# Optimization experiments

Hardware: AMD Instinct MI355X
Metric: run time of the kernel (lower is better)

The kernel has to match this reference:

```python
import jax, jax.numpy as jnp
import numpy as np

B, T, E, H, VF, C = 4, 8192, 512, 8, 2, 256
KD = E // H          # key dim per head = 64
HD = E * VF // H     # value head dim = 128


def _rel_pos():
    decay = np.log(1.0 - 2.0 ** (-5.0 - np.arange(H, dtype=np.float64)))  # [H]
    ang = 1.0 / (10000 ** np.linspace(0, 1, KD // 2))
    ang = np.repeat(ang, 2)                                  # [KD]
    idx = np.arange(T)
    sin = np.sin(idx[:, None] * ang[None, :]).astype(np.float32)
    cos = np.cos(idx[:, None] * ang[None, :]).astype(np.float32)
    bi = np.arange(C)
    diff = bi[:, None] - bi[None, :]
    m = np.where(diff >= 0, np.exp(decay[:, None, None] * diff), 0.0)  # [H,C,C]
    last = m[:, -1]                                          # [H,C]
    vid = (last / last.sum(-1, keepdims=True))[:, :, None]   # [H,C,1]
    scale = np.sqrt(m.sum(-1, keepdims=True))                # [H,C,1]
    mask = (m / scale).astype(np.float32)
    cross_decay = np.exp(decay * C)[:, None, None].astype(np.float32)  # [H,1,1]
    qid = np.exp(decay[:, None] * (bi + 1))[:, :, None]      # [H,C,1]
    qid = (qid / (scale / last.sum(-1)[:, None, None])).astype(np.float32)
    return sin, cos, mask, cross_decay, qid, vid.astype(np.float32)


def setup_inputs() -> dict:
    key = jax.random.key(0)
    ks = jax.random.split(key, 6)
    sin, cos, mask, cross_decay, qid, vid = _rel_pos()
    s = 0.02
    return {
        'x': jax.random.normal(ks[0], (B, T, E), jnp.float32),
        'sin': jnp.asarray(sin), 'cos': jnp.asarray(cos),
        'mask': jnp.asarray(mask), 'cross_decay': jnp.asarray(cross_decay),
        'query_inner_decay': jnp.asarray(qid), 'value_inner_decay': jnp.asarray(vid),
        'Wq': jax.random.normal(ks[1], (E, E), jnp.float32) * s,
        'Wk': jax.random.normal(ks[2], (E, E), jnp.float32) * s,
        'Wv': jax.random.normal(ks[3], (E, E * VF), jnp.float32) * s,
        'Wg': jax.random.normal(ks[4], (E, E * VF), jnp.float32) * s,
        'Wo': jax.random.normal(ks[5], (E * VF, E), jnp.float32) * s,
    }


def _rotate_every_two(x):
    x1, x2 = x[..., ::2], x[..., 1::2]
    return jnp.stack((-x2, x1), axis=-1).reshape(x.shape)


def _theta_shift(x, sin, cos):
    return x * cos + _rotate_every_two(x) * sin


def reference(x, sin, cos, mask, cross_decay, query_inner_decay, value_inner_decay, Wq, Wk, Wv, Wg, Wo):
    Bz, Tl, _ = x.shape
    q = (x @ Wq).reshape(Bz, Tl, H, KD).transpose(0, 2, 1, 3)               # [B,H,T,KD]
    k = ((x @ Wk) * (KD ** -0.5)).reshape(Bz, Tl, H, KD).transpose(0, 2, 1, 3)
    v = x @ Wv                                                              # [B,T,E*VF]
    g = x @ Wg
    qr = _theta_shift(q, sin, cos)
    kr = _theta_shift(k, sin, cos)

    NC = Tl // C
    qr = qr.reshape(Bz, H, NC, C, KD).transpose(0, 2, 1, 3, 4)              # [B,NC,H,C,KD]
    kr = kr.reshape(Bz, H, NC, C, KD).transpose(0, 2, 1, 3, 4)
    vc = v.reshape(Bz, NC, C, H, HD).transpose(0, 1, 3, 2, 4)               # [B,NC,H,C,HD]

    qk = jnp.einsum('bnhck,bnhdk->bnhcd', qr, kr) * mask                    # decay-masked intra-chunk
    inner_scale = jnp.clip(jax.lax.stop_gradient(jnp.abs(qk)).sum(-1, keepdims=True), 1.0, None)
    qk = qk / inner_scale
    inner_output = jnp.einsum('bnhcd,bnhde->bnhce', qk, vc)                 # [B,NC,H,C,HD]

    kv = jnp.einsum('bnhck,bnhcd->bnhkd', kr, vc * value_inner_decay)       # [B,NC,H,KD,HD]

    def step(carry, kv_i):
        kv_state, kv_scale = carry
        out = (kv_state / kv_scale, kv_scale)
        kv_state = kv_state * cross_decay + kv_i
        kv_scale = jnp.clip(
            jax.lax.stop_gradient(jnp.abs(kv_state)).sum(-2, keepdims=True).max(-1, keepdims=True),
            1.0, None)
        return (kv_state, kv_scale), out

    kv_state0 = jnp.zeros((Bz, H, KD, HD), x.dtype)
    kv_scale0 = jnp.ones((Bz, H, 1, 1), x.dtype)
    _, (kv_recurrent, cross_scale) = jax.lax.scan(step, (kv_state0, kv_scale0), jnp.swapaxes(kv, 0, 1))
    kv_recurrent = jnp.swapaxes(kv_recurrent, 0, 1)                         # [B,NC,H,KD,HD]
    cross_scale = jnp.swapaxes(cross_scale, 0, 1)                           # [B,NC,H,1,1]

    all_scale = jnp.maximum(inner_scale, cross_scale)
    cross_output = jnp.einsum('bnhck,bnhkd->bnhcd', qr * query_inner_decay, kv_recurrent)
    output = inner_output / (all_scale / inner_scale) + cross_output / (all_scale / cross_scale)
    output = output.transpose(0, 1, 3, 2, 4)                                # [B,NC,C,H,HD]
    # group_norm: RMSNorm over head_dim, no affine
    output = output * jax.lax.rsqrt(jnp.mean(output ** 2, -1, keepdims=True) + 1e-6)
    output = output.reshape(Bz, Tl, H * HD)
    output = jax.nn.silu(g) * output
    return output @ Wo
```

## Files before the change

### kernel.cpp

```cpp
#include <hip/hip_runtime.h>
#include <cmath>

#define Bz 4
#define Tt 8192
#define Ee 512
#define Hh 8
#define Cc 256
#define KD 64
#define HD 128
#define NC 32
#define EV 1024
#define Mrows (Bz*Tt)

typedef unsigned short u16;
typedef __attribute__((ext_vector_type(4))) float f32x4;
typedef __attribute__((ext_vector_type(8))) short s16x8;

__device__ __forceinline__ u16 f2b(float f) {
    union { float f; unsigned u; } v; v.f = f;
    unsigned r = v.u + 0x7FFFu + ((v.u >> 16) & 1u);
    return (u16)(r >> 16);
}
__device__ __forceinline__ float b2f(u16 u) {
    union { unsigned u; float f; } v; v.u = ((unsigned)u) << 16;
    return v.f;
}
#define MFMA16(a, b, c) __builtin_amdgcn_mfma_f32_16x16x32_bf16((a), (b), (c), 0, 0, 0)

__device__ __forceinline__ void glds16(const u16* g, u16* l) {
    __builtin_amdgcn_global_load_lds(
        (const __attribute__((address_space(1))) unsigned int*)g,
        (__attribute__((address_space(3))) unsigned int*)l,
        16, 0, 0);
}

__device__ __forceinline__ size_t fpk(int row, int k, int K) {
    return (size_t)(row >> 4) * (K * 16) + (k >> 5) * 512 + ((k >> 3) & 3) * 128 +
           (row & 15) * 8 + (k & 7);
}

__global__ __launch_bounds__(256) void cast_x_k(const float* __restrict__ x,
                                                u16* __restrict__ xb) {
    size_t i = ((size_t)blockIdx.x * 256 + threadIdx.x) * 4;
    float4 v = *(const float4*)(x + i);
    int m = (int)(i >> 9), e = (int)(i & 511);
    ushort4 o;
    o.x = f2b(v.x); o.y = f2b(v.y); o.z = f2b(v.z); o.w = f2b(v.w);
    *(ushort4*)(xb + fpk(m, e, 512)) = o;
}

__global__ __launch_bounds__(256) void castT_k(const float* __restrict__ W,
                                               u16* __restrict__ Wt,
                                               int K, int N, float scale) {
    __shared__ float tile[32][33];
    int k0 = blockIdx.y * 32, n0 = blockIdx.x * 32;
    int r = threadIdx.x >> 3, c4 = (threadIdx.x & 7) * 4;
    float4 v = *(const float4*)(W + (size_t)(k0 + r) * N + n0 + c4);
    tile[r][c4] = v.x; tile[r][c4 + 1] = v.y; tile[r][c4 + 2] = v.z; tile[r][c4 + 3] = v.w;
    __syncthreads();
    ushort4 o;
    o.x = f2b(tile[c4 + 0][r] * scale);
    o.y = f2b(tile[c4 + 1][r] * scale);
    o.z = f2b(tile[c4 + 2][r] * scale);
    o.w = f2b(tile[c4 + 3][r] * scale);
    *(ushort4*)(Wt + fpk(n0 + r, k0 + c4, K)) = o;
}

template <int EPI>
__global__ __launch_bounds__(256) void gemm_mfma(const u16* __restrict__ A,
                                                 const u16* __restrict__ Bt,
                                                 void* __restrict__ Cout,
                                                 int K, int N,
                                                 const float* __restrict__ sn,
                                                 const float* __restrict__ cs) {
    __shared__ __align__(16) u16 pool[20480];
    u16 (*lds)[8192] = (u16(*)[8192])pool;
    int tid = threadIdx.x;
    int lane = tid & 63, wid = tid >> 6;
    int cL = lane & 15, quad = lane >> 4;
    int M0 = blockIdx.y * 8, N0 = blockIdx.x * 8;
    int m0 = blockIdx.y * 128 + (wid & 1) * 64;
    int n0 = blockIdx.x * 128 + (wid >> 1) * 64;
    const int KT = K * 16;
    const int NK = K >> 5;

#define STAGE(buf, kc) do {                                                        \
        size_t kofs = (size_t)(kc) * 512 + lane * 8;                               \
        glds16(A  + (size_t)(M0 + wid * 2    ) * KT + kofs,                        \
               &lds[buf][(wid * 2    ) * 512]);                                    \
        glds16(A  + (size_t)(M0 + wid * 2 + 1) * KT + kofs,                        \
               &lds[buf][(wid * 2 + 1) * 512]);                                    \
        glds16(Bt + (size_t)(N0 + wid * 2    ) * KT + kofs,                        \
               &lds[buf][4096 + (wid * 2    ) * 512]);                             \
        glds16(Bt + (size_t)(N0 + wid * 2 + 1) * KT + kofs,                        \
               &lds[buf][4096 + (wid * 2 + 1) * 512]);                             \
    } while (0)

    STAGE(0, 0);
    __syncthreads();

    f32x4 acc[4][4] = {};
    int mh = (wid & 1) * 4, nh = (wid >> 1) * 4;
    for (int kc = 0; kc < NK; ++kc) {
        int cur = kc & 1;
        if (kc + 1 < NK) STAGE(cur ^ 1, kc + 1);
        s16x8 af[4], bfr[4];
        int fo = quad * 128 + cL * 8;
        #pragma unroll
        for (int mt = 0; mt < 4; ++mt)
            af[mt] = *(const s16x8*)(&lds[cur][(mh + mt) * 512 + fo]);
        #pragma unroll
        for (int nt = 0; nt < 4; ++nt)
            bfr[nt] = *(const s16x8*)(&lds[cur][4096 + (nh + nt) * 512 + fo]);
        #pragma unroll
        for (int mt = 0; mt < 4; ++mt)
            #pragma unroll
            for (int nt = 0; nt < 4; ++nt)
                acc[mt][nt] = MFMA16(af[mt], bfr[nt], acc[mt][nt]);
        __syncthreads();
    }
#undef STAGE
    u16* ep = pool + wid * 5120;

    if (EPI == 0) {
        u16* dst = (u16*)Cout;
        int b = m0 >> 13, h = n0 >> 6, tb = m0 & 8191;
        #pragma unroll
        for (int mt = 0; mt < 4; ++mt)
            #pragma unroll
            for (int nt = 0; nt < 4; ++nt)
                #pragma unroll
                for (int i = 0; i < 4; ++i) {
                    int mrow = mt * 16 + quad * 4 + i;
                    int n = n0 + nt * 16 + cL;
                    float v = acc[mt][nt][i];
                    float p = __shfl_xor(v, 1, 64);
                    int t = tb + mrow, kd = n & 63;
                    float c1 = cs[t * 64 + kd], s1 = sn[t * 64 + kd];
                    float o = (n & 1) ? (v * c1 + p * s1) : (v * c1 - p * s1);
                    ep[mrow * 80 + nt * 16 + cL] = f2b(o);
                }
        u16* dstbh = dst + (size_t)(b * 8 + h) * 524288;
        #pragma unroll
        for (int g2 = 0; g2 < 4; ++g2)
            #pragma unroll
            for (int pass = 0; pass < 2; ++pass) {
                int kcol = pass * 32 + quad * 8;
                s16x8 vv = *(const s16x8*)(ep + (g2 * 16 + cL) * 80 + kcol);
                *(s16x8*)(dstbh + fpk(tb + g2 * 16 + cL, kcol, 64)) = vv;
            }
    } else if (EPI == 1) {
        u16* vt = (u16*)Cout;
        #pragma unroll
        for (int mt = 0; mt < 4; ++mt)
            #pragma unroll
            for (int nt = 0; nt < 4; ++nt) {
                int m = m0 + mt * 16 + quad * 4;
                int n = n0 + nt * 16 + cL;
                int b = m >> 13, t = m & 8191;
                int nn = t >> 8, ccc = t & 255;
                int h = n >> 7, e = n & 127;
                ushort4 pk;
                pk.x = f2b(acc[mt][nt][0]);
                pk.y = f2b(acc[mt][nt][1]);
                pk.z = f2b(acc[mt][nt][2]);
                pk.w = f2b(acc[mt][nt][3]);
                *(ushort4*)(vt + (((size_t)((b * 8 + h) * 32 + nn)) << 15) +
                            fpk(e, ccc, 256)) = pk;
            }
    } else if (EPI == 2) {
        u16* dst = (u16*)Cout;
        #pragma unroll
        for (int mt = 0; mt < 4; ++mt)
            #pragma unroll
            for (int nt = 0; nt < 4; ++nt)
                #pragma unroll
                for (int i = 0; i < 4; ++i)
                    ep[(mt * 16 + quad * 4 + i) * 80 + nt * 16 + cL] =
                        f2b(acc[mt][nt][i]);
        #pragma unroll
        for (int g2 = 0; g2 < 4; ++g2)
            #pragma unroll
            for (int pass = 0; pass < 2; ++pass) {
                int ncol = pass * 32 + quad * 8;
                s16x8 vv = *(const s16x8*)(ep + (g2 * 16 + cL) * 80 + ncol);
                *(s16x8*)(dst + fpk(m0 + g2 * 16 + cL, n0 + ncol, N)) = vv;
            }
    } else {
        float* dst = (float*)Cout;
        #pragma unroll
        for (int mt = 0; mt < 4; ++mt)
            #pragma unroll
            for (int nt = 0; nt < 4; ++nt)
                #pragma unroll
                for (int i = 0; i < 4; ++i)
                    dst[(size_t)(m0 + mt * 16 + quad * 4 + i) * N + n0 + nt * 16 + cL] =
                        acc[mt][nt][i];
    }
}

__global__ __launch_bounds__(256) void attn_mfma(const u16* __restrict__ qr,
                                                 const u16* __restrict__ kr,
                                                 const u16* __restrict__ vt,
                                                 const float* __restrict__ mask,
                                                 u16* __restrict__ ATT,
                                                 float* __restrict__ iscale_g) {
    __shared__ __align__(16) u16 Ss[64][264];
    __shared__ float partial[4][64];
    __shared__ float sInvL[64];
    int p = blockIdx.x;
    int g = (p & 7) | ((p >> 5) << 3);
    int rtile = (p >> 3) & 3;
    int h = g & 7; int n = (g >> 3) & 31; int b = g >> 8;
    int tid = threadIdx.x, lane = tid & 63, w = tid >> 6;
    int cL = lane & 15, quad = lane >> 4;

    size_t qf_bh = (size_t)(b * 8 + h) * 524288;
    f32x4 acc[4][4] = {};
    if (w <= rtile) {
        const u16* Qb = qr + qf_bh + (size_t)(n * 16 + rtile * 4) * 1024;
        const u16* Kb = kr + qf_bh + (size_t)(n * 16 + w * 4) * 1024;
        #pragma unroll
        for (int kt = 0; kt < 2; ++kt) {
            s16x8 af[4], bfr[4];
            size_t ko = (size_t)kt * 512 + quad * 128 + cL * 8;
            #pragma unroll
            for (int mt = 0; mt < 4; ++mt)
                af[mt] = *(const s16x8*)(Qb + (size_t)mt * 1024 + ko);
            #pragma unroll
            for (int nt = 0; nt < 4; ++nt)
                bfr[nt] = *(const s16x8*)(Kb + (size_t)nt * 1024 + ko);
            #pragma unroll
            for (int mt = 0; mt < 4; ++mt)
                #pragma unroll
                for (int nt = 0; nt < 4; ++nt)
                    acc[mt][nt] = MFMA16(af[mt], bfr[nt], acc[mt][nt]);
        }
    }
    float rs[4][4] = {};
    if (w <= rtile) {
        const float* mb = mask + ((size_t)h << 16);
        #pragma unroll
        for (int mt = 0; mt < 4; ++mt)
            #pragma unroll
            for (int nt = 0; nt < 4; ++nt)
                #pragma unroll
                for (int i = 0; i < 4; ++i) {
                    int r = rtile * 64 + mt * 16 + quad * 4 + i;
                    int d = w * 64 + nt * 16 + cL;
                    float s = acc[mt][nt][i] * mb[r * 256 + d];
                    Ss[mt * 16 + quad * 4 + i][w * 64 + nt * 16 + cL] = f2b(s);
                    rs[mt][i] += fabsf(s);
                }
    }
    #pragma unroll
    for (int mt = 0; mt < 4; ++mt)
        #pragma unroll
        for (int i = 0; i < 4; ++i) {
            float v = rs[mt][i];
            v += __shfl_xor(v, 1, 16);
            v += __shfl_xor(v, 2, 16);
            v += __shfl_xor(v, 4, 16);
            v += __shfl_xor(v, 8, 16);
            if (cL == 0) partial[w][mt * 16 + quad * 4 + i] = v;
        }
    __syncthreads();
    if (tid < 64) {
        float tot = partial[0][tid] + partial[1][tid] + partial[2][tid] + partial[3][tid];
        tot = fmaxf(tot, 1.f);
        iscale_g[((size_t)((b * 32 + n) * 8 + h)) * 256 + rtile * 64 + tid] = tot;
        sInvL[tid] = 1.f / tot;
    }
    __syncthreads();

    f32x4 o[8] = {};
    const u16* Vb = vt + (((size_t)((b * 8 + h) * 32 + n)) << 15);
    int kmax = 2 * (rtile + 1);
    for (int kt = 0; kt < kmax; ++kt) {
        s16x8 a = *(const s16x8*)(&Ss[w * 16 + cL][kt * 32 + quad * 8]);
        #pragma unroll
        for (int nt = 0; nt < 8; ++nt) {
            s16x8 bv = *(const s16x8*)(Vb + (size_t)nt * 4096 + kt * 512 +
                                       quad * 128 + cL * 8);
            o[nt] = MFMA16(a, bv, o[nt]);
        }
    }
    #pragma unroll
    for (int nt = 0; nt < 8; ++nt)
        #pragma unroll
        for (int i = 0; i < 4; ++i) {
            int r = quad * 4 + i;
            Ss[w * 16 + r][nt * 16 + cL] = f2b(o[nt][i] * sInvL[w * 16 + r]);
        }
    size_t obase = ((size_t)b * 8192 + n * 256 + rtile * 64) * 1024 + h * 128;
    #pragma unroll
    for (int pass = 0; pass < 4; ++pass) {
        int e = pass * 32 + quad * 8;
        s16x8 vv = *(const s16x8*)(&Ss[w * 16 + cL][e]);
        *(s16x8*)(ATT + obase + (size_t)(w * 16 + cL) * 1024 + e) = vv;
    }
}

__global__ __launch_bounds__(256) void chunkkv_mfma(const u16* __restrict__ kr,
                                                    const u16* __restrict__ vt,
                                                    const float* __restrict__ vid,
                                                    float* __restrict__ kvT) {
    __shared__ u16 KtL[64][264];
    int bid = blockIdx.x;
    int h = bid & 7; bid >>= 3;
    int n = bid & 31; int b = bid >> 5;
    int tid = threadIdx.x, lane = tid & 63, w = tid >> 6;
    int cL = lane & 15, quad = lane >> 4;
    size_t qf_bh = (size_t)(b * 8 + h) * 524288;
    {
        int c = tid;
        const u16* rp = kr + qf_bh + (size_t)(n * 16 + (c >> 4)) * 1024 + (c & 15) * 8;
        #pragma unroll
        for (int u = 0; u < 8; ++u) {
            s16x8 vv = *(const s16x8*)(rp + (u >> 2) * 512 + (u & 3) * 128);
            #pragma unroll
            for (int j = 0; j < 8; ++j) KtL[u * 8 + j][c] = (u16)vv[j];
        }
    }
    __syncthreads();
    const u16* Vb = vt + (((size_t)((b * 8 + h) * 32 + n)) << 15);
    f32x4 acc[2][4] = {};
    for (int kt = 0; kt < 8; ++kt) {
        float vidv[8];
        #pragma unroll
        for (int j = 0; j < 8; ++j) vidv[j] = vid[h * 256 + kt * 32 + quad * 8 + j];
        s16x8 af[2];
        #pragma unroll
        for (int mt = 0; mt < 2; ++mt) {
            s16x8 raw = *(const s16x8*)(Vb + (size_t)(w * 2 + mt) * 4096 +
                                        kt * 512 + quad * 128 + cL * 8);
            #pragma unroll
            for (int j = 0; j < 8; ++j)
                af[mt][j] = (short)f2b(b2f((u16)raw[j]) * vidv[j]);
        }
        #pragma unroll
        for (int nt = 0; nt < 4; ++nt) {
            s16x8 bv = *(const s16x8*)(&KtL[nt * 16 + cL][kt * 32 + quad * 8]);
            #pragma unroll
            for (int mt = 0; mt < 2; ++mt) acc[mt][nt] = MFMA16(af[mt], bv, acc[mt][nt]);
        }
    }
    float* out = kvT + ((size_t)((b * 32 + n) * 8 + h)) * 8192;
    #pragma unroll
    for (int mt = 0; mt < 2; ++mt)
        #pragma unroll
        for (int nt = 0; nt < 4; ++nt)
            #pragma unroll
            for (int i = 0; i < 4; ++i)
                out[(w * 32 + mt * 16 + quad * 4 + i) * 64 + nt * 16 + cL] = acc[mt][nt][i];
}

__global__ __launch_bounds__(256) void scan_par(const float* __restrict__ kvT,
                                                u16* __restrict__ kvrecb,
                                                const float* __restrict__ cdv,
                                                float* __restrict__ cscale) {
    int bid = blockIdx.x;
    int n = bid & 31; bid >>= 5;
    int h = bid & 7; int b = bid >> 3;
    int tid = threadIdx.x, lane = tid & 63, g = tid >> 6;
    float cd = cdv[h];
    float st[32];
    #pragma unroll
    for (int i = 0; i < 32; ++i) st[i] = 0.f;
    for (int j = 0; j < n; ++j) {
        size_t base = ((size_t)((b * 32 + j) * 8 + h)) * 8192;
        #pragma unroll
        for (int i = 0; i < 32; ++i) {
            int e = g + 4 * i;
            st[i] = st[i] * cd + kvT[base + e * 64 + lane];
        }
    }
    __shared__ float esum[128];
    __shared__ float sSc;
    #pragma unroll
    for (int i = 0; i < 32; ++i) {
        float s = fabsf(st[i]);
        s += __shfl_xor(s, 1, 64);
        s += __shfl_xor(s, 2, 64);
        s += __shfl_xor(s, 4, 64);
        s += __shfl_xor(s, 8, 64);
        s += __shfl_xor(s, 16, 64);
        s += __shfl_xor(s, 32, 64);
        if (lane == 0) esum[g + 4 * i] = s;
    }
    __syncthreads();
    if (tid < 64) {
        float m1 = fmaxf(esum[tid], esum[tid + 64]);
        m1 = fmaxf(m1, __shfl_xor(m1, 1, 64));
        m1 = fmaxf(m1, __shfl_xor(m1, 2, 64));
        m1 = fmaxf(m1, __shfl_xor(m1, 4, 64));
        m1 = fmaxf(m1, __shfl_xor(m1, 8, 64));
        m1 = fmaxf(m1, __shfl_xor(m1, 16, 64));
        m1 = fmaxf(m1, __shfl_xor(m1, 32, 64));
        if (tid == 0) sSc = fmaxf(m1, 1.f);
    }
    __syncthreads();
    float scale = sSc;
    float inv = 1.f / scale;
    size_t baseN = ((size_t)((b * 32 + n) * 8 + h)) * 8192;
    #pragma unroll
    for (int i = 0; i < 32; ++i) {
        int e = g + 4 * i;
        kvrecb[baseN + ((size_t)(lane >> 3) * 128 + e) * 8 + (lane & 7)] = f2b(st[i] * inv);
    }
    if (tid == 0) cscale[(b * 32 + n) * 8 + h] = scale;
}

__global__ __launch_bounds__(256) void cross_mfma(const u16* __restrict__ qr,
                                                  const u16* __restrict__ kvrecb,
                                                  const float* __restrict__ iscale_g,
                                                  const float* __restrict__ cscale_g,
                                                  const float* __restrict__ qid,
                                                  u16* __restrict__ ATT) {
    __shared__ __align__(16) u16 X[4][4608];
    int bid = blockIdx.x;
    int h = bid & 7; bid >>= 3;
    int n = bid & 31; int b = bid >> 5;
    int tid = threadIdx.x, lane = tid & 63, w = tid >> 6;
    int cL = lane & 15, quad = lane >> 4;
    size_t qf_bh = (size_t)(b * 8 + h) * 524288;
    const u16* Qb = qr + qf_bh + (size_t)(n * 16 + w * 4) * 1024;
    const u16* KVb = kvrecb + ((size_t)((b * 32 + n) * 8 + h)) * 8192;
    s16x8 af[4][2];
    #pragma unroll
    for (int mt = 0; mt < 4; ++mt)
        #pragma unroll
        for (int kt = 0; kt < 2; ++kt)
            af[mt][kt] = *(const s16x8*)(Qb + (size_t)mt * 1024 + kt * 512 +
                                         quad * 128 + cL * 8);
    float csc = cscale_g[(b * 32 + n) * 8 + h];
    size_t ibase = ((size_t)((b * 32 + n) * 8 + h)) * 256 + w * 64;
    size_t obase = ((size_t)(b * 8192 + n * 256 + w * 64)) * 1024 + h * 128;
    #pragma unroll
    for (int hn = 0; hn < 2; ++hn) {
        f32x4 acc[4][4] = {};
        #pragma unroll
        for (int kt = 0; kt < 2; ++kt)
            #pragma unroll
            for (int nt = 0; nt < 4; ++nt) {
                int e = (hn * 4 + nt) * 16 + cL;
                s16x8 bv = *(const s16x8*)(KVb + ((size_t)(kt * 4 + quad) * 128 + e) * 8);
                #pragma unroll
                for (int mt = 0; mt < 4; ++mt)
                    acc[mt][nt] = MFMA16(af[mt][kt], bv, acc[mt][nt]);
            }
        #pragma unroll
        for (int mt = 0; mt < 4; ++mt)
            #pragma unroll
            for (int i = 0; i < 4; ++i) {
                int r = mt * 16 + quad * 4 + i;
                float isc = iscale_g[ibase + r];
                float alls = fmaxf(isc, csc);
                float fC = (csc / alls) * qid[h * 256 + w * 64 + r];
                #pragma unroll
                for (int nt = 0; nt < 4; ++nt)
                    X[w][r * 72 + nt * 16 + cL] = f2b(acc[mt][nt][i] * fC);
            }
        #pragma unroll
        for (int g2 = 0; g2 < 4; ++g2)
            #pragma unroll
            for (int pass = 0; pass < 2; ++pass) {
                int r2 = g2 * 16 + cL;
                float isc2 = iscale_g[ibase + r2];
                float fI2 = isc2 / fmaxf(isc2, csc);
                int e = pass * 32 + quad * 8;
                s16x8 sv = *(const s16x8*)(&X[w][r2 * 72 + e]);
                size_t oi = obase + (size_t)r2 * 1024 + hn * 64 + e;
                s16x8 pv = *(const s16x8*)(ATT + oi);
                s16x8 ov;
                #pragma unroll
                for (int j = 0; j < 8; ++j)
                    ov[j] = (short)f2b(b2f((u16)pv[j]) * fI2 + b2f((u16)sv[j]));
                *(s16x8*)(ATT + oi) = ov;
            }
    }
}

__global__ __launch_bounds__(256) void rms_silu(const u16* __restrict__ ATT,
                                                u16* __restrict__ g) {
    __shared__ u16 att_s[16 * 1036];
    __shared__ float rmsv[16][8];
    int tile = blockIdx.x;
    int tid = threadIdx.x;
    size_t abase = (size_t)tile * 16 * 1024;
    int head = tid >> 5;
    #pragma unroll
    for (int jj = 0; jj < 16; ++jj) {
        ushort4 v = *(const ushort4*)(ATT + abase + (size_t)jj * 1024 + tid * 4);
        *(ushort4*)(att_s + jj * 1036 + tid * 4) = v;
        float x0 = b2f(v.x), x1 = b2f(v.y), x2 = b2f(v.z), x3 = b2f(v.w);
        float ss = x0 * x0 + x1 * x1 + x2 * x2 + x3 * x3;
        ss += __shfl_xor(ss, 1, 32);
        ss += __shfl_xor(ss, 2, 32);
        ss += __shfl_xor(ss, 4, 32);
        ss += __shfl_xor(ss, 8, 32);
        ss += __shfl_xor(ss, 16, 32);
        if ((tid & 31) == 0)
            rmsv[jj][head] = rsqrtf(ss * (1.f / 128.f) + 1e-6f);
    }
    __syncthreads();
    size_t gbase = (size_t)tile * 16384;
    #pragma unroll
    for (int it = 0; it < 16; ++it) {
        int p = it * 1024 + tid * 4;
        int e = ((p >> 9) << 5) | (((p >> 7) & 3) << 3) | (p & 7);
        int r = (p >> 3) & 15;
        ushort4 gv = *(const ushort4*)(g + gbase + p);
        ushort4 av = *(const ushort4*)(att_s + r * 1036 + e);
        float rms = rmsv[r][e >> 7];
        float x0 = b2f(av.x), x1 = b2f(av.y), x2 = b2f(av.z), x3 = b2f(av.w);
        float g0 = b2f(gv.x), g1 = b2f(gv.y), g2 = b2f(gv.z), g3 = b2f(gv.w);
        ushort4 ov;
        ov.x = f2b((g0 / (1.f + __expf(-g0))) * x0 * rms);
        ov.y = f2b((g1 / (1.f + __expf(-g1))) * x1 * rms);
        ov.z = f2b((g2 / (1.f + __expf(-g2))) * x2 * rms);
        ov.w = f2b((g3 / (1.f + __expf(-g3))) * x3 * rms);
        *(ushort4*)(g + gbase + p) = ov;
    }
}

extern "C" void kernel_launch(void* const* d_in, const int* in_sizes, int n_in,
                              void* d_out, int out_size, void* d_ws, size_t ws_size,
                              hipStream_t stream) {
    const float* x    = (const float*)d_in[0];
    const float* sn   = (const float*)d_in[1];
    const float* cs   = (const float*)d_in[2];
    const float* mask = (const float*)d_in[3];
    const float* cdv  = (const float*)d_in[4];
    const float* qid  = (const float*)d_in[5];
    const float* vid  = (const float*)d_in[6];
    const float* Wq   = (const float*)d_in[7];
    const float* Wk   = (const float*)d_in[8];
    const float* Wv   = (const float*)d_in[9];
    const float* Wg   = (const float*)d_in[10];
    const float* Wo   = (const float*)d_in[11];
    float* out = (float*)d_out;

    char* w = (char*)d_ws;
    u16* qr     = (u16*)w;   w += (size_t)16777216 * 2;
    u16* kr     = (u16*)w;   w += (size_t)16777216 * 2;
    u16* vt     = (u16*)w;   w += (size_t)33554432 * 2;
    u16* xbf    = (u16*)w;   w += (size_t)16777216 * 2;
    u16* wqT    = (u16*)w;   w += (size_t)262144 * 2;
    u16* wkT    = (u16*)w;   w += (size_t)262144 * 2;
    u16* wvT    = (u16*)w;   w += (size_t)524288 * 2;
    u16* wgT    = (u16*)w;   w += (size_t)524288 * 2;
    u16* woT    = (u16*)w;   w += (size_t)524288 * 2;
    float* kvT  = (float*)w; w += (size_t)8388608 * 4;
    u16* kvrecb = (u16*)w;   w += (size_t)8388608 * 2;
    float* iscale = (float*)w; w += (size_t)262144 * 4;
    float* cscale = (float*)w; w += (size_t)1024 * 4;

    u16* gbuf = qr;
    u16* ATT  = (u16*)d_out;

    dim3 blk(256);
    cast_x_k<<<dim3(16384), blk, 0, stream>>>(x, xbf);
    castT_k<<<dim3(16, 16), blk, 0, stream>>>(Wq, wqT, 512, 512, 1.0f);
    castT_k<<<dim3(16, 16), blk, 0, stream>>>(Wk, wkT, 512, 512, 0.125f);
    castT_k<<<dim3(32, 16), blk, 0, stream>>>(Wv, wvT, 512, 1024, 1.0f);
    castT_k<<<dim3(32, 16), blk, 0, stream>>>(Wg, wgT, 512, 1024, 1.0f);
    castT_k<<<dim3(16, 32), blk, 0, stream>>>(Wo, woT, 1024, 512, 1.0f);
    gemm_mfma<0><<<dim3(4, 256), blk, 0, stream>>>(xbf, wqT, qr, 512, 512, sn, cs);
    gemm_mfma<0><<<dim3(4, 256), blk, 0, stream>>>(xbf, wkT, kr, 512, 512, sn, cs);
    gemm_mfma<1><<<dim3(8, 256), blk, 0, stream>>>(xbf, wvT, vt, 512, 1024, nullptr, nullptr);
    attn_mfma<<<dim3(4096), blk, 0, stream>>>(qr, kr, vt, mask, ATT, iscale);
    chunkkv_mfma<<<dim3(1024), blk, 0, stream>>>(kr, vt, vid, kvT);
    scan_par<<<dim3(1024), blk, 0, stream>>>(kvT, kvrecb, cdv, cscale);
    cross_mfma<<<dim3(1024), blk, 0, stream>>>(qr, kvrecb, iscale, cscale, qid, ATT);
    gemm_mfma<2><<<dim3(8, 256), blk, 0, stream>>>(xbf, wgT, gbuf, 512, 1024, nullptr, nullptr);
    rms_silu<<<dim3(2048), blk, 0, stream>>>(ATT, gbuf);
    gemm_mfma<3><<<dim3(4, 256), blk, 0, stream>>>(gbuf, woT, out, 1024, 512, nullptr, nullptr);
}
```

Measured before the change: 647.3 us.

## Fuse RMSNorm+SiLU gating into gate GEMM epilogue, bf16 mask, prefetch scan loads

Removes the separate rms_silu kernel by computing the per-head RMS normalization and SiLU gating inside the Wg GEMM epilogue, staging the gate tile through LDS. This avoids writing and re-reading the gate buffer. The mask is also pre-cast to bf16 so attention reads half the bytes, and the scan kernel software-prefetches the next chunk's state. These add an extra cast kernel, some mask precision loss, and more registers in the scan kernel.

```diff
diff --git a/kernel.cpp b/kernel.cpp
--- a/kernel.cpp
+++ b/kernel.cpp
@@ -49,6 +49,15 @@
     *(ushort4*)(xb + fpk(m, e, 512)) = o;
 }
 
+__global__ __launch_bounds__(256) void cast_mask_k(const float* __restrict__ m,
+                                                   u16* __restrict__ mb) {
+    size_t i = ((size_t)blockIdx.x * 256 + threadIdx.x) * 4;
+    float4 v = *(const float4*)(m + i);
+    ushort4 o;
+    o.x = f2b(v.x); o.y = f2b(v.y); o.z = f2b(v.z); o.w = f2b(v.w);
+    *(ushort4*)(mb + i) = o;
+}
+
 __global__ __launch_bounds__(256) void castT_k(const float* __restrict__ W,
                                                u16* __restrict__ Wt,
                                                int K, int N, float scale) {
@@ -72,7 +81,8 @@
                                                  void* __restrict__ Cout,
                                                  int K, int N,
                                                  const float* __restrict__ sn,
-                                                 const float* __restrict__ cs) {
+                                                 const float* __restrict__ cs,
+                                                 const u16* __restrict__ att) {
     __shared__ __align__(16) u16 pool[20480];
     u16 (*lds)[8192] = (u16(*)[8192])pool;
     int tid = threadIdx.x;
@@ -168,24 +178,55 @@
                 *(ushort4*)(vt + (((size_t)((b * 8 + h) * 32 + nn)) << 15) +
                             fpk(e, ccc, 256)) = pk;
             }
-    } else if (EPI == 2) {
+    } else if (EPI == 4) {
         u16* dst = (u16*)Cout;
-        #pragma unroll
-        for (int mt = 0; mt < 4; ++mt)
-            #pragma unroll
-            for (int nt = 0; nt < 4; ++nt)
-                #pragma unroll
-                for (int i = 0; i < 4; ++i)
-                    ep[(mt * 16 + quad * 4 + i) * 80 + nt * 16 + cL] =
-                        f2b(acc[mt][nt][i]);
-        #pragma unroll
-        for (int g2 = 0; g2 < 4; ++g2)
-            #pragma unroll
-            for (int pass = 0; pass < 2; ++pass) {
-                int ncol = pass * 32 + quad * 8;
-                s16x8 vv = *(const s16x8*)(ep + (g2 * 16 + cL) * 80 + ncol);
-                *(s16x8*)(dst + fpk(m0 + g2 * 16 + cL, n0 + ncol, N)) = vv;
-            }
+        int mb0 = blockIdx.y * 128;
+        int h = blockIdx.x;
+        u16* eps = pool;
+        int rl = lane >> 4, c16 = lane & 15;
+        #pragma unroll
+        for (int ph = 0; ph < 2; ++ph) {
+            __syncthreads();
+            if ((wid & 1) == ph) {
+                #pragma unroll
+                for (int mt = 0; mt < 4; ++mt)
+                    #pragma unroll
+                    for (int nt = 0; nt < 4; ++nt)
+                        #pragma unroll
+                        for (int i = 0; i < 4; ++i)
+                            eps[(mt * 16 + quad * 4 + i) * 138 +
+                                (wid >> 1) * 64 + nt * 16 + cL] = f2b(acc[mt][nt][i]);
+            }
+            __syncthreads();
+            #pragma unroll
+            for (int it = 0; it < 4; ++it) {
+                int row = wid * 16 + it * 4 + rl;
+                int grow = mb0 + ph * 64 + row;
+                size_t arow = (size_t)grow * 1024 + h * 128 + c16 * 8;
+                s16x8 av = *(const s16x8*)(att + arow);
+                s16x8 gv = *(const s16x8*)(eps + row * 138 + c16 * 8);
+                float afv[8], gfv[8];
+                float ssq = 0.f;
+                #pragma unroll
+                for (int j = 0; j < 8; ++j) {
+                    afv[j] = b2f((u16)av[j]);
+                    gfv[j] = b2f((u16)gv[j]);
+                    ssq += afv[j] * afv[j];
+                }
+                ssq += __shfl_xor(ssq, 1, 16);
+                ssq += __shfl_xor(ssq, 2, 16);
+                ssq += __shfl_xor(ssq, 4, 16);
+                ssq += __shfl_xor(ssq, 8, 16);
+                float rms = rsqrtf(ssq * (1.f / 128.f) + 1e-6f);
+                s16x8 ov;
+                #pragma unroll
+                for (int j = 0; j < 8; ++j) {
+                    float sg = gfv[j] / (1.f + __expf(-gfv[j]));
+                    ov[j] = (short)f2b(sg * afv[j] * rms);
+                }
+                *(s16x8*)(dst + fpk(grow, h * 128 + c16 * 8, N)) = ov;
+            }
+        }
     } else {
         float* dst = (float*)Cout;
         #pragma unroll
@@ -202,7 +243,7 @@
 __global__ __launch_bounds__(256) void attn_mfma(const u16* __restrict__ qr,
                                                  const u16* __restrict__ kr,
                                                  const u16* __restrict__ vt,
-                                                 const float* __restrict__ mask,
+                                                 const u16* __restrict__ maskb,
                                                  u16* __restrict__ ATT,
                                                  float* __restrict__ iscale_g) {
     __shared__ __align__(16) u16 Ss[64][264];
@@ -239,7 +280,7 @@
     }
     float rs[4][4] = {};
     if (w <= rtile) {
-        const float* mb = mask + ((size_t)h << 16);
+        const u16* mb = maskb + ((size_t)h << 16);
         #pragma unroll
         for (int mt = 0; mt < 4; ++mt)
             #pragma unroll
@@ -248,7 +289,7 @@
                 for (int i = 0; i < 4; ++i) {
                     int r = rtile * 64 + mt * 16 + quad * 4 + i;
                     int d = w * 64 + nt * 16 + cL;
-                    float s = acc[mt][nt][i] * mb[r * 256 + d];
+                    float s = acc[mt][nt][i] * b2f(mb[r * 256 + d]);
                     Ss[mt * 16 + quad * 4 + i][w * 64 + nt * 16 + cL] = f2b(s);
                     rs[mt][i] += fabsf(s);
                 }
@@ -364,16 +405,24 @@
     int h = bid & 7; int b = bid >> 3;
     int tid = threadIdx.x, lane = tid & 63, g = tid >> 6;
     float cd = cdv[h];
-    float st[32];
-    #pragma unroll
-    for (int i = 0; i < 32; ++i) st[i] = 0.f;
+    float st[32], cur[32], nxt[32];
+    #pragma unroll
+    for (int i = 0; i < 32; ++i) { st[i] = 0.f; nxt[i] = 0.f; }
+    if (n > 0) {
+        size_t base0 = ((size_t)((b * 32) * 8 + h)) * 8192;
+        #pragma unroll
+        for (int i = 0; i < 32; ++i) cur[i] = kvT[base0 + (g + 4 * i) * 64 + lane];
+    }
     for (int j = 0; j < n; ++j) {
-        size_t base = ((size_t)((b * 32 + j) * 8 + h)) * 8192;
-        #pragma unroll
-        for (int i = 0; i < 32; ++i) {
-            int e = g + 4 * i;
-            st[i] = st[i] * cd + kvT[base + e * 64 + lane];
-        }
+        if (j + 1 < n) {
+            size_t basen = ((size_t)((b * 32 + j + 1) * 8 + h)) * 8192;
+            #pragma unroll
+            for (int i = 0; i < 32; ++i) nxt[i] = kvT[basen + (g + 4 * i) * 64 + lane];
+        }
+        #pragma unroll
+        for (int i = 0; i < 32; ++i) st[i] = st[i] * cd + cur[i];
+        #pragma unroll
+        for (int i = 0; i < 32; ++i) cur[i] = nxt[i];
     }
     __shared__ float esum[128];
     __shared__ float sSc;
@@ -481,49 +530,6 @@
     }
 }
 
-__global__ __launch_bounds__(256) void rms_silu(const u16* __restrict__ ATT,
-                                                u16* __restrict__ g) {
-    __shared__ u16 att_s[16 * 1036];
-    __shared__ float rmsv[16][8];
-    int tile = blockIdx.x;
-    int tid = threadIdx.x;
-    size_t abase = (size_t)tile * 16 * 1024;
-    int head = tid >> 5;
-    #pragma unroll
-    for (int jj = 0; jj < 16; ++jj) {
-        ushort4 v = *(const ushort4*)(ATT + abase + (size_t)jj * 1024 + tid * 4);
-        *(ushort4*)(att_s + jj * 1036 + tid * 4) = v;
-        float x0 = b2f(v.x), x1 = b2f(v.y), x2 = b2f(v.z), x3 = b2f(v.w);
-        float ss = x0 * x0 + x1 * x1 + x2 * x2 + x3 * x3;
-        ss += __shfl_xor(ss, 1, 32);
-        ss += __shfl_xor(ss, 2, 32);
-        ss += __shfl_xor(ss, 4, 32);
-        ss += __shfl_xor(ss, 8, 32);
-        ss += __shfl_xor(ss, 16, 32);
-        if ((tid & 31) == 0)
-            rmsv[jj][head] = rsqrtf(ss * (1.f / 128.f) + 1e-6f);
-    }
-    __syncthreads();
-    size_t gbase = (size_t)tile * 16384;
-    #pragma unroll
-    for (int it = 0; it < 16; ++it) {
-        int p = it * 1024 + tid * 4;
-        int e = ((p >> 9) << 5) | (((p >> 7) & 3) << 3) | (p & 7);
-        int r = (p >> 3) & 15;
-        ushort4 gv = *(const ushort4*)(g + gbase + p);
-        ushort4 av = *(const ushort4*)(att_s + r * 1036 + e);
-        float rms = rmsv[r][e >> 7];
-        float x0 = b2f(av.x), x1 = b2f(av.y), x2 = b2f(av.z), x3 = b2f(av.w);
-        float g0 = b2f(gv.x), g1 = b2f(gv.y), g2 = b2f(gv.z), g3 = b2f(gv.w);
-        ushort4 ov;
-        ov.x = f2b((g0 / (1.f + __expf(-g0))) * x0 * rms);
-        ov.y = f2b((g1 / (1.f + __expf(-g1))) * x1 * rms);
-        ov.z = f2b((g2 / (1.f + __expf(-g2))) * x2 * rms);
-        ov.w = f2b((g3 / (1.f + __expf(-g3))) * x3 * rms);
-        *(ushort4*)(g + gbase + p) = ov;
-    }
-}
-
 extern "C" void kernel_launch(void* const* d_in, const int* in_sizes, int n_in,
                               void* d_out, int out_size, void* d_ws, size_t ws_size,
                               hipStream_t stream) {
@@ -555,25 +561,26 @@
     u16* kvrecb = (u16*)w;   w += (size_t)8388608 * 2;
     float* iscale = (float*)w; w += (size_t)262144 * 4;
     float* cscale = (float*)w; w += (size_t)1024 * 4;
+    u16* maskb  = (u16*)w;   w += (size_t)524288 * 2;
 
     u16* gbuf = qr;
     u16* ATT  = (u16*)d_out;
 
     dim3 blk(256);
     cast_x_k<<<dim3(16384), blk, 0, stream>>>(x, xbf);
+    cast_mask_k<<<dim3(512), blk, 0, stream>>>(mask, maskb);
     castT_k<<<dim3(16, 16), blk, 0, stream>>>(Wq, wqT, 512, 512, 1.0f);
     castT_k<<<dim3(16, 16), blk, 0, stream>>>(Wk, wkT, 512, 512, 0.125f);
     castT_k<<<dim3(32, 16), blk, 0, stream>>>(Wv, wvT, 512, 1024, 1.0f);
     castT_k<<<dim3(32, 16), blk, 0, stream>>>(Wg, wgT, 512, 1024, 1.0f);
     castT_k<<<dim3(16, 32), blk, 0, stream>>>(Wo, woT, 1024, 512, 1.0f);
-    gemm_mfma<0><<<dim3(4, 256), blk, 0, stream>>>(xbf, wqT, qr, 512, 512, sn, cs);
-    gemm_mfma<0><<<dim3(4, 256), blk, 0, stream>>>(xbf, wkT, kr, 512, 512, sn, cs);
-    gemm_mfma<1><<<dim3(8, 256), blk, 0, stream>>>(xbf, wvT, vt, 512, 1024, nullptr, nullptr);
-    attn_mfma<<<dim3(4096), blk, 0, stream>>>(qr, kr, vt, mask, ATT, iscale);
+    gemm_mfma<0><<<dim3(4, 256), blk, 0, stream>>>(xbf, wqT, qr, 512, 512, sn, cs, nullptr);
+    gemm_mfma<0><<<dim3(4, 256), blk, 0, stream>>>(xbf, wkT, kr, 512, 512, sn, cs, nullptr);
+    gemm_mfma<1><<<dim3(8, 256), blk, 0, stream>>>(xbf, wvT, vt, 512, 1024, nullptr, nullptr, nullptr);
+    attn_mfma<<<dim3(4096), blk, 0, stream>>>(qr, kr, vt, maskb, ATT, iscale);
     chunkkv_mfma<<<dim3(1024), blk, 0, stream>>>(kr, vt, vid, kvT);
     scan_par<<<dim3(1024), blk, 0, stream>>>(kvT, kvrecb, cdv, cscale);
     cross_mfma<<<dim3(1024), blk, 0, stream>>>(qr, kvrecb, iscale, cscale, qid, ATT);
-    gemm_mfma<2><<<dim3(8, 256), blk, 0, stream>>>(xbf, wgT, gbuf, 512, 1024, nullptr, nullptr);
-    rms_silu<<<dim3(2048), blk, 0, stream>>>(ATT, gbuf);
-    gemm_mfma<3><<<dim3(4, 256), blk, 0, stream>>>(gbuf, woT, out, 1024, 512, nullptr, nullptr);
-}
+    gemm_mfma<4><<<dim3(8, 256), blk, 0, stream>>>(xbf, wgT, gbuf, 512, 1024, nullptr, nullptr, ATT);
+    gemm_mfma<3><<<dim3(4, 256), blk, 0, stream>>>(gbuf, woT, out, 1024, 512, nullptr, nullptr, nullptr);
+}
```

After: 685.9 us. +6.0%, slower.
